# Kernel tuning notes

Hardware: AMD Instinct MI355X
Metric: run time of the kernel (lower is better)

## Reference

```python
import jax, jax.numpy as jnp
import numpy as np

N = 100_000   # nodes
E = 1_600_000 # edges (avg degree 16)
G = 1_000     # graphs in batch
IN = 3
H = 64
EPS = 1e-5    # BatchNorm eps


def setup_inputs() -> dict:
    key = jax.random.key(0)
    ks = jax.random.split(key, 16)
    x = jax.random.normal(ks[0], (N, IN), jnp.float32)
    edge_index = jax.random.randint(ks[1], (2, E), 0, N, dtype=jnp.int64)
    # sorted segment ids covering every graph (no empty segments for max-pool)
    batch = (jnp.arange(N, dtype=jnp.int64) * G) // N
    s = 0.1
    return {
        "x": x,
        "edge_index": edge_index,
        "batch": batch,
        "W0": jax.random.normal(ks[2], (IN, H), jnp.float32) * s,
        "b0": jax.random.normal(ks[3], (H,), jnp.float32) * s,
        "W_hidden": jax.random.normal(ks[4], (2, H, H), jnp.float32) * s,
        "b_hidden": jax.random.normal(ks[5], (2, H), jnp.float32) * s,
        "bn_gamma": jax.random.uniform(ks[6], (3, H), jnp.float32, 0.5, 1.5),
        "bn_beta": jax.random.normal(ks[7], (3, H), jnp.float32) * s,
        "bn_mean": jax.random.normal(ks[8], (3, H), jnp.float32) * s,
        "bn_var": jax.random.uniform(ks[9], (3, H), jnp.float32, 0.5, 1.5),
        "fc1_W": jax.random.normal(ks[10], (2 * H, 128), jnp.float32) * s,
        "fc1_b": jnp.zeros((128,), jnp.float32),
        "fc2_W": jax.random.normal(ks[11], (128, 64), jnp.float32) * s,
        "fc2_b": jnp.zeros((64,), jnp.float32),
        "fcg_W": jax.random.normal(ks[12], (64, 1), jnp.float32) * s,
        "fcg_b": jnp.zeros((1,), jnp.float32),
        "fcb_W": jax.random.normal(ks[13], (64, 1), jnp.float32) * s,
        "fcb_b": jnp.zeros((1,), jnp.float32),
    }


def _gcn_conv(h, W, b, src, dst, dinv):
    """PyG GCNConv: self-loops + symmetric deg^{-1/2} normalization."""
    hw = h @ W                                   # [N, out]
    norm = dinv[src] * dinv[dst]                 # [E]
    agg = jax.ops.segment_sum(hw[src] * norm[:, None], dst, num_segments=N)
    # self-loop contribution: norm_ii = dinv_i^2
    return agg + hw * (dinv * dinv)[:, None] + b


def reference(x, edge_index, batch, W0, b0, W_hidden, b_hidden,
              bn_gamma, bn_beta, bn_mean, bn_var,
              fc1_W, fc1_b, fc2_W, fc2_b, fcg_W, fcg_b, fcb_W, fcb_b):
    src, dst = edge_index[0], edge_index[1]
    # degree including self-loop, computed on target nodes (PyG gcn_norm)
    deg = jax.ops.segment_sum(jnp.ones((E,), x.dtype), dst, num_segments=N) + 1.0
    dinv = jax.lax.rsqrt(deg)

    h = x
    for i in range(3):
        W = W0 if i == 0 else W_hidden[i - 1]
        b = b0 if i == 0 else b_hidden[i - 1]
        hn = _gcn_conv(h, W, b, src, dst, dinv)
        # BatchNorm1d (eval mode, running stats) + ReLU; dropout = identity in eval
        hn = (hn - bn_mean[i]) * jax.lax.rsqrt(bn_var[i] + EPS) * bn_gamma[i] + bn_beta[i]
        hn = jax.nn.relu(hn)
        h = h + hn if (i > 0 and h.shape[1] == hn.shape[1]) else hn

    # segment pooling over graphs
    counts = jax.ops.segment_sum(jnp.ones((N,), h.dtype), batch, num_segments=G)
    x_mean = jax.ops.segment_sum(h, batch, num_segments=G) / counts[:, None]
    x_max = jax.ops.segment_max(h, batch, num_segments=G)
    g = jnp.concatenate([x_mean, x_max], axis=1)     # [G, 2H]

    g = jax.nn.relu(g @ fc1_W + fc1_b)
    g = jax.nn.relu(g @ fc2_W + fc2_b)
    gamma = g @ fcg_W + fcg_b
    beta = g @ fcb_W + fcb_b
    return jnp.concatenate([gamma, beta], axis=1)    # [G, 2*p_layers]
```

## Files before the change

kernel.cpp:

```cpp
#include <hip/hip_runtime.h>
#include <hip/hip_fp16.h>
#include <math.h>
#include <float.h>

#define EPSBN 1e-5f
#define NBK   200
#define CAPB  9728
#define STGB  64
#define BATCH 4096

typedef _Float16 f16x8 __attribute__((ext_vector_type(8)));
typedef float f32x4 __attribute__((ext_vector_type(4)));


__global__ void prep(const float* __restrict__ W, __half* __restrict__ Whi,
                     __half* __restrict__ Wlo, int n, int* __restrict__ cursors) {
    int i = blockIdx.x * 256 + threadIdx.x;
    if (blockIdx.x == 0 && threadIdx.x < NBK) cursors[threadIdx.x] = 0;
    if (i < n) {
        float w = W[i];
        __half hi = __float2half_rn(w);
        float rem = w - __half2float(hi);
        Whi[i] = hi;
        Wlo[i] = __float2half_rn(rem);
    }
}

__global__ void bin_edges(const int* __restrict__ src, const int* __restrict__ dst,
                          int* __restrict__ bufs, int* __restrict__ cursors,
                          int E, int N) {
    __shared__ int stage[NBK * STGB];
    __shared__ int cnt[NBK];
    __shared__ int bpos[NBK];
    int tid = threadIdx.x;
    int nb = (N + 511) >> 9;

    int chunk = (((E + gridDim.x - 1) / gridDim.x) + 3) & ~3;
    int e0 = blockIdx.x * chunk;
    int e1 = min(e0 + chunk, E);

    for (int base = e0; base < e1; base += BATCH) {
        for (int i = tid; i < NBK; i += 512) cnt[i] = 0;
        __syncthreads();

#pragma unroll
        for (int it = 0; it < 2; it++) {
            int e = base + it * 2048 + tid * 4;
            if (e + 4 <= e1) {
                int4 d4 = *(const int4*)(dst + e);
                int4 s4 = *(const int4*)(src + e);
                int dd[4] = {d4.x, d4.y, d4.z, d4.w};
                int ss[4] = {s4.x, s4.y, s4.z, s4.w};
#pragma unroll
                for (int q = 0; q < 4; q++) {
                    int d = dd[q];
                    int b = d >> 9;
                    int w = ((d & 511) << 17) | ss[q];
                    int pos = atomicAdd(&cnt[b], 1);
                    if (pos < STGB) stage[b * STGB + pos] = w;
                }
            } else {
                for (int qq = e; qq < e1 && qq < e + 4; qq++) {
                    int d = dst[qq];
                    int b = d >> 9;
                    int w = ((d & 511) << 17) | src[qq];
                    int pos = atomicAdd(&cnt[b], 1);
                    if (pos < STGB) stage[b * STGB + pos] = w;
                }
            }
        }
        __syncthreads();
        if (tid < nb) bpos[tid] = atomicAdd(&cursors[tid], min(cnt[tid], STGB));
        __syncthreads();
        int wv = tid >> 6, ln = tid & 63;
        for (int b = wv; b < nb; b += 8) {
            int c = min(cnt[b], STGB), bp = bpos[b];
            int* dstp = bufs + (size_t)b * CAPB + bp;
            for (int i = ln; i < c; i += 64)
                if (bp + i < CAPB) dstp[i] = stage[b * STGB + i];
        }
        __syncthreads();
    }
}

__global__ void __launch_bounds__(512)
build_csr(const int* __restrict__ bufs, const int* __restrict__ cursors,
          const float* __restrict__ x,
          float* __restrict__ dinv, float* __restrict__ xs,
          int* __restrict__ off0, int* __restrict__ off1,
          int* __restrict__ csr, int N) {
    __shared__ int cnt[512];
    __shared__ int pfx[512];
    __shared__ unsigned sorted[CAPB];
    int tid = threadIdx.x;
    int b = blockIdx.x;
    cnt[tid] = 0;
    __syncthreads();
    int total = min(cursors[b], CAPB);
    const int* buf = bufs + (size_t)b * CAPB;

    for (int i = tid * 4; i + 4 <= total; i += 2048) {
        int4 w4 = *(const int4*)(buf + i);
        atomicAdd(&cnt[w4.x >> 17], 1);
        atomicAdd(&cnt[w4.y >> 17], 1);
        atomicAdd(&cnt[w4.z >> 17], 1);
        atomicAdd(&cnt[w4.w >> 17], 1);
    }
    for (int i = (total & ~3) + tid; i < total; i += 512)
        atomicAdd(&cnt[buf[i] >> 17], 1);
    __syncthreads();

    int v = cnt[tid];
    pfx[tid] = v;
    __syncthreads();
    for (int off = 1; off < 512; off <<= 1) {
        int t = (tid >= off) ? pfx[tid - off] : 0;
        __syncthreads();
        pfx[tid] += t;
        __syncthreads();
    }
    int excl = pfx[tid] - v;
    int gbase = b * CAPB;
    int gi = (b << 9) + tid;
    if (gi < N) {
        float di = 1.0f / sqrtf((float)v + 1.0f);
        dinv[gi] = di;
        off0[gi] = gbase + excl;
        off1[gi] = gbase + excl + v;
        xs[gi * 3]     = x[gi * 3]     * di;
        xs[gi * 3 + 1] = x[gi * 3 + 1] * di;
        xs[gi * 3 + 2] = x[gi * 3 + 2] * di;
    }
    cnt[tid] = excl;
    __syncthreads();

    for (int i = tid * 4; i + 4 <= total; i += 2048) {
        int4 w4 = *(const int4*)(buf + i);
        int ww[4] = {w4.x, w4.y, w4.z, w4.w};
#pragma unroll
        for (int q = 0; q < 4; q++) {
            int pos = atomicAdd(&cnt[ww[q] >> 17], 1);
            sorted[pos] = (unsigned)(ww[q] & 0x1FFFF);
        }
    }
    for (int i = (total & ~3) + tid; i < total; i += 512) {
        int w = buf[i];
        int pos = atomicAdd(&cnt[w >> 17], 1);
        sorted[pos] = (unsigned)(w & 0x1FFFF);
    }
    __syncthreads();

    for (int i = tid; i < total; i += 512)
        csr[gbase + i] = (int)sorted[i];
}

__global__ void agg3(const float* __restrict__ xs, const float* __restrict__ dinv,
                     const int* __restrict__ csr,
                     const int* __restrict__ off0, const int* __restrict__ off1,
                     float* __restrict__ ax, int N) {
    int n = blockIdx.x * blockDim.x + threadIdx.x;
    if (n >= N) return;
    float a0 = xs[n * 3], a1 = xs[n * 3 + 1], a2 = xs[n * 3 + 2];
    float b0 = 0.f, b1 = 0.f, b2 = 0.f;
    int e0 = off0[n], e1 = off1[n];
    int e = e0;
    for (; e + 4 <= e1; e += 4) {
        int s0 = csr[e] * 3, s1 = csr[e + 1] * 3, s2 = csr[e + 2] * 3, s3 = csr[e + 3] * 3;
        float x00 = xs[s0], x01 = xs[s0 + 1], x02 = xs[s0 + 2];
        float x10 = xs[s1], x11 = xs[s1 + 1], x12 = xs[s1 + 2];
        float x20 = xs[s2], x21 = xs[s2 + 1], x22 = xs[s2 + 2];
        float x30 = xs[s3], x31 = xs[s3 + 1], x32 = xs[s3 + 2];
        a0 += x00 + x20; a1 += x01 + x21; a2 += x02 + x22;
        b0 += x10 + x30; b1 += x11 + x31; b2 += x12 + x32;
    }
    for (; e < e1; e++) {
        int s = csr[e] * 3;
        a0 += xs[s]; a1 += xs[s + 1]; a2 += xs[s + 2];
    }
    float di = dinv[n];
    ax[n * 3]     = (a0 + b0) * di;
    ax[n * 3 + 1] = (a1 + b1) * di;
    ax[n * 3 + 2] = (a2 + b2) * di;
}

__global__ void mm_bn(const float* __restrict__ ax, const float* __restrict__ W,
                      const float* __restrict__ b,
                      const float* __restrict__ bng, const float* __restrict__ bnb,
                      const float* __restrict__ bnm, const float* __restrict__ bnv,
                      __half* __restrict__ h, int N) {
    int t = blockIdx.x * blockDim.x + threadIdx.x;
    int n = t >> 6, f = t & 63;
    if (n < N) {
        float a = ax[n * 3] * W[f] + ax[n * 3 + 1] * W[64 + f]
                + ax[n * 3 + 2] * W[128 + f] + b[f];
        float v = (a - bnm[f]) * rsqrtf(bnv[f] + EPSBN) * bng[f] + bnb[f];
        v = fmaxf(v, 0.f);
        float other = __shfl_xor(v, 1, 64);
        if (!(f & 1)) ((__half2*)h)[t >> 1] = __floats2half2_rn(v, other);
    }
}

__global__ void __launch_bounds__(256)
mm64_mfma(const __half* __restrict__ hH, const __half* __restrict__ WhiH,
          const __half* __restrict__ WloH, const float* __restrict__ dinv,
          __half* __restrict__ hw, int N) {
    __shared__ _Float16 lds[4][16 * 68];
    const _Float16* Whi = (const _Float16*)WhiH;
    const _Float16* Wlo = (const _Float16*)WloH;
    const _Float16* hh  = (const _Float16*)hH;

    int tid = threadIdx.x;
    int lane = tid & 63;
    int wv = tid >> 6;
    int col = lane & 15;
    int q = lane >> 4;
    int gwave = blockIdx.x * 4 + wv;
    int nwaves = gridDim.x * 4;
    int ntiles = (N + 15) >> 4;

    f16x8 Bh[2][4], Bl[2][4];
#pragma unroll
    for (int t = 0; t < 2; t++)
#pragma unroll
        for (int g = 0; g < 4; g++) {
#pragma unroll
            for (int j = 0; j < 8; j++) {
                int k = t * 32 + q * 8 + j;
                Bh[t][g][j] = Whi[k * 64 + g * 16 + col];
                Bl[t][g][j] = Wlo[k * 64 + g * 16 + col];
            }
        }

    _Float16* sl = lds[wv];

    for (int tile = gwave; tile < ntiles; tile += nwaves) {
        int base = tile << 4;
        int arow = base + col;
        if (arow > N - 1) arow = N - 1;
        f32x4 acc[4] = {};
#pragma unroll
        for (int t = 0; t < 2; t++) {
            f16x8 a = *(const f16x8*)(hh + (size_t)arow * 64 + t * 32 + q * 8);
#pragma unroll
            for (int g = 0; g < 4; g++) {
                acc[g] = __builtin_amdgcn_mfma_f32_16x16x32_f16(a, Bh[t][g], acc[g], 0, 0, 0);
                acc[g] = __builtin_amdgcn_mfma_f32_16x16x32_f16(a, Bl[t][g], acc[g], 0, 0, 0);
            }
        }
#pragma unroll
        for (int r = 0; r < 4; r++) {
            int row = base + q * 4 + r;
            float di = dinv[row < N ? row : N - 1];
#pragma unroll
            for (int g = 0; g < 4; g++)
                sl[(q * 4 + r) * 68 + g * 16 + col] = (_Float16)(acc[g][r] * di);
        }
        asm volatile("s_waitcnt lgkmcnt(0)" ::: "memory");
#pragma unroll
        for (int p = 0; p < 2; p++) {
            int row = (lane >> 3) + p * 8;
            int ck = lane & 7;
            uint4 v = *(const uint4*)(sl + row * 68 + ck * 8);
            int grow = base + row;
            if (grow < N)
                *(uint4*)(hw + (size_t)grow * 64 + ck * 8) = v;
        }
        asm volatile("s_waitcnt lgkmcnt(0)" ::: "memory");
    }
}


__device__ inline void acc8(float* a, uint4 r) {
    const __half2* p = (const __half2*)&r;
#pragma unroll
    for (int j = 0; j < 4; j++) {
        float2 f = __half22float2(p[j]);
        a[2 * j] += f.x;
        a[2 * j + 1] += f.y;
    }
}

__global__ void agg_bn(const uint4* __restrict__ hw4, __half* __restrict__ h,
                       const float* __restrict__ dinv,
                       const int* __restrict__ csr,
                       const int* __restrict__ off0, const int* __restrict__ off1,
                       const float4* __restrict__ bias4,
                       const float4* __restrict__ gamma4, const float4* __restrict__ beta4,
                       const float4* __restrict__ mean4, const float4* __restrict__ var4,
                       int N) {
    int tid = threadIdx.x;
    int n = blockIdx.x * 32 + (tid >> 3);
    int f8 = tid & 7;
    if (n >= N) return;

    float a0[8], a1[8], a2[8], a3[8];
#pragma unroll
    for (int j = 0; j < 8; j++) { a0[j] = 0.f; a1[j] = 0.f; a2[j] = 0.f; a3[j] = 0.f; }
    acc8(a0, hw4[(size_t)n * 8 + f8]);

    int e0 = off0[n], e1 = off1[n];
    int e = e0;
    for (; e + 16 <= e1; e += 16) {
        int s[16];
#pragma unroll
        for (int j = 0; j < 16; j++) s[j] = csr[e + j];
        uint4 v[16];
#pragma unroll
        for (int j = 0; j < 16; j++) v[j] = hw4[(size_t)s[j] * 8 + f8];
#pragma unroll
        for (int j = 0; j < 16; j += 4) {
            acc8(a0, v[j]); acc8(a1, v[j + 1]); acc8(a2, v[j + 2]); acc8(a3, v[j + 3]);
        }
    }
    for (; e + 4 <= e1; e += 4) {
        int s0 = csr[e], s1 = csr[e + 1], s2 = csr[e + 2], s3 = csr[e + 3];
        uint4 v0 = hw4[(size_t)s0 * 8 + f8];
        uint4 v1 = hw4[(size_t)s1 * 8 + f8];
        uint4 v2 = hw4[(size_t)s2 * 8 + f8];
        uint4 v3 = hw4[(size_t)s3 * 8 + f8];
        acc8(a0, v0); acc8(a1, v1); acc8(a2, v2); acc8(a3, v3);
    }
    for (; e < e1; e++)
        acc8(a0, hw4[(size_t)csr[e] * 8 + f8]);

    float di = dinv[n];
    float4 bA = bias4[f8 * 2],  bB = bias4[f8 * 2 + 1];
    float4 gA = gamma4[f8 * 2], gB = gamma4[f8 * 2 + 1];
    float4 eA = beta4[f8 * 2],  eB = beta4[f8 * 2 + 1];
    float4 mA = mean4[f8 * 2],  mB = mean4[f8 * 2 + 1];
    float4 vA = var4[f8 * 2],   vB = var4[f8 * 2 + 1];
    float bb[8] = {bA.x, bA.y, bA.z, bA.w, bB.x, bB.y, bB.z, bB.w};
    float gg[8] = {gA.x, gA.y, gA.z, gA.w, gB.x, gB.y, gB.z, gB.w};
    float ee[8] = {eA.x, eA.y, eA.z, eA.w, eB.x, eB.y, eB.z, eB.w};
    float mm[8] = {mA.x, mA.y, mA.z, mA.w, mB.x, mB.y, mB.z, mB.w};
    float vv[8] = {vA.x, vA.y, vA.z, vA.w, vB.x, vB.y, vB.z, vB.w};

    float r[8];
#pragma unroll
    for (int j = 0; j < 8; j++) {
        float acc = (a0[j] + a1[j]) + (a2[j] + a3[j]);
        float t = (acc * di + bb[j] - mm[j]) * (1.0f / sqrtf(vv[j] + EPSBN)) * gg[j] + ee[j];
        r[j] = fmaxf(t, 0.f);
    }
    {
        uint4 hp = ((const uint4*)h)[(size_t)n * 8 + f8];
        const __half2* pp = (const __half2*)&hp;
#pragma unroll
        for (int j = 0; j < 4; j++) {
            float2 f = __half22float2(pp[j]);
            r[2 * j] += f.x;
            r[2 * j + 1] += f.y;
        }
    }
    uint4 outv;
    __half2* po = (__half2*)&outv;
#pragma unroll
    for (int j = 0; j < 4; j++) po[j] = __floats2half2_rn(r[2 * j], r[2 * j + 1]);
    ((uint4*)h)[(size_t)n * 8 + f8] = outv;
}


__device__ inline float4 h4_to_f4(uint2 r) {
    __half2 a = *(__half2*)&r.x;
    __half2 b = *(__half2*)&r.y;
    float2 fa = __half22float2(a), fb = __half22float2(b);
    return make_float4(fa.x, fa.y, fb.x, fb.y);
}

__global__ void __launch_bounds__(256)
pool_mlp(const uint2* __restrict__ h2, const int* __restrict__ batch, int N,
         const float* __restrict__ W1, const float* __restrict__ b1,
         const float* __restrict__ W2, const float* __restrict__ b2,
         const float* __restrict__ Wg, const float* __restrict__ bg,
         const float* __restrict__ Wb, const float* __restrict__ bbv,
         float* __restrict__ out) {
    __shared__ float4 ssum[256], smax[256];
    __shared__ float pooled[128];
    __shared__ float h1[128], hh2[64];
    __shared__ int range[2];
    int g = blockIdx.x;
    int tid = threadIdx.x;

    if (tid < 2) {
        int target = g + tid;
        int lo = 0, hi = N;
        while (lo < hi) {
            int mid = (lo + hi) >> 1;
            if (batch[mid] < target) lo = mid + 1; else hi = mid;
        }
        range[tid] = lo;
    }
    __syncthreads();
    int s = range[0], e = range[1];

    int f4 = tid & 15, c = tid >> 4;
    float4 sum = make_float4(0.f, 0.f, 0.f, 0.f);
    float4 mx = make_float4(-FLT_MAX, -FLT_MAX, -FLT_MAX, -FLT_MAX);
    for (int i = s + c; i < e; i += 16) {
        float4 v = h4_to_f4(h2[(size_t)i * 16 + f4]);
        sum.x += v.x; sum.y += v.y; sum.z += v.z; sum.w += v.w;
        mx.x = fmaxf(mx.x, v.x); mx.y = fmaxf(mx.y, v.y);
        mx.z = fmaxf(mx.z, v.z); mx.w = fmaxf(mx.w, v.w);
    }
    ssum[tid] = sum;
    smax[tid] = mx;
    __syncthreads();
    for (int half = 8; half >= 1; half >>= 1) {
        if (c < half) {
            int o = tid + half * 16;
            ssum[tid].x += ssum[o].x; ssum[tid].y += ssum[o].y;
            ssum[tid].z += ssum[o].z; ssum[tid].w += ssum[o].w;
            smax[tid].x = fmaxf(smax[tid].x, smax[o].x);
            smax[tid].y = fmaxf(smax[tid].y, smax[o].y);
            smax[tid].z = fmaxf(smax[tid].z, smax[o].z);
            smax[tid].w = fmaxf(smax[tid].w, smax[o].w);
        }
        __syncthreads();
    }
    if (c == 0) {
        float inv = 1.0f / (float)(e - s);
        float4 S = ssum[tid], M = smax[tid];
        pooled[f4 * 4 + 0] = S.x * inv;
        pooled[f4 * 4 + 1] = S.y * inv;
        pooled[f4 * 4 + 2] = S.z * inv;
        pooled[f4 * 4 + 3] = S.w * inv;
        pooled[64 + f4 * 4 + 0] = M.x;
        pooled[64 + f4 * 4 + 1] = M.y;
        pooled[64 + f4 * 4 + 2] = M.z;
        pooled[64 + f4 * 4 + 3] = M.w;
    }
    __syncthreads();

    if (tid < 128) {
        float acc = b1[tid];
#pragma unroll 8
        for (int k = 0; k < 128; k++) acc += pooled[k] * W1[k * 128 + tid];
        h1[tid] = fmaxf(acc, 0.0f);
    }
    __syncthreads();
    if (tid < 64) {
        float a2 = b2[tid];
#pragma unroll 8
        for (int k = 0; k < 128; k++) a2 += h1[k] * W2[k * 64 + tid];
        hh2[tid] = fmaxf(a2, 0.0f);
    }
    __syncthreads();
    if (tid < 2) {
        const float* Wv = (tid == 0) ? Wg : Wb;
        float a = (tid == 0) ? bg[0] : bbv[0];
        for (int k = 0; k < 64; k++) a += hh2[k] * Wv[k];
        out[g * 2 + tid] = a;
    }
}


extern "C" void kernel_launch(void* const* d_in, const int* in_sizes, int n_in,
                              void* d_out, int out_size, void* d_ws, size_t ws_size,
                              hipStream_t stream) {
    const float* x    = (const float*)d_in[0];
    const int*   ei   = (const int*)d_in[1];
    const int*   batch= (const int*)d_in[2];
    const float* W0   = (const float*)d_in[3];
    const float* b0   = (const float*)d_in[4];
    const float* Wh   = (const float*)d_in[5];
    const float* bh   = (const float*)d_in[6];
    const float* bng  = (const float*)d_in[7];
    const float* bnb  = (const float*)d_in[8];
    const float* bnm  = (const float*)d_in[9];
    const float* bnv  = (const float*)d_in[10];
    const float* fc1W = (const float*)d_in[11];
    const float* fc1b = (const float*)d_in[12];
    const float* fc2W = (const float*)d_in[13];
    const float* fc2b = (const float*)d_in[14];
    const float* fcgW = (const float*)d_in[15];
    const float* fcgb = (const float*)d_in[16];
    const float* fcbW = (const float*)d_in[17];
    const float* fcbb = (const float*)d_in[18];
    float* out = (float*)d_out;

    const int N = in_sizes[0] / 3;
    const int E = in_sizes[1] / 2;
    const int G = out_size / 2;
    const int* src = ei;
    const int* dst = ei + E;
    const int nb = (N + 511) >> 9;

    char* ws = (char*)d_ws;
    auto alloc = [&](size_t bytes) {
        char* p = ws;
        ws += (bytes + 255) & ~(size_t)255;
        return p;
    };
    float*  dinv    = (float*)alloc((size_t)N * 4);
    int*    off0    = (int*)alloc((size_t)N * 4);
    int*    off1    = (int*)alloc((size_t)N * 4);
    int*    csr     = (int*)alloc((size_t)NBK * CAPB * 4);
    int*    bufs    = (int*)alloc((size_t)NBK * CAPB * 4);
    int*    cursors = (int*)alloc(NBK * 4);
    float*  xs      = (float*)alloc((size_t)N * 3 * 4);
    float*  ax      = (float*)alloc((size_t)N * 3 * 4);
    __half* h       = (__half*)alloc((size_t)N * 64 * 2);
    __half* hw      = (__half*)alloc((size_t)N * 64 * 2);
    __half* whi     = (__half*)alloc(2 * 4096 * 2);
    __half* wlo     = (__half*)alloc(2 * 4096 * 2);

    const int B = 256;

    prep<<<32, 256, 0, stream>>>(Wh, whi, wlo, 8192, cursors);
    bin_edges<<<768, 512, 0, stream>>>(src, dst, bufs, cursors, E, N);
    build_csr<<<nb, 512, 0, stream>>>(bufs, cursors, x, dinv, xs, off0, off1, csr, N);

    int aggBlocks = (N + 31) / 32;

    agg3<<<(N + B - 1) / B, B, 0, stream>>>(xs, dinv, csr, off0, off1, ax, N);
    mm_bn<<<((size_t)N * 64 + B - 1) / B, B, 0, stream>>>(ax, W0, b0,
                                                          bng, bnb, bnm, bnv, h, N);
    mm64_mfma<<<784, 256, 0, stream>>>(h, whi, wlo, dinv, hw, N);
    agg_bn<<<aggBlocks, 256, 0, stream>>>((const uint4*)hw, h, dinv, csr, off0, off1,
                                          (const float4*)(bh),
                                          (const float4*)(bng + 64), (const float4*)(bnb + 64),
                                          (const float4*)(bnm + 64), (const float4*)(bnv + 64), N);
    mm64_mfma<<<784, 256, 0, stream>>>(h, whi + 4096, wlo + 4096, dinv, hw, N);
    agg_bn<<<aggBlocks, 256, 0, stream>>>((const uint4*)hw, h, dinv, csr, off0, off1,
                                          (const float4*)(bh + 64),
                                          (const float4*)(bng + 128), (const float4*)(bnb + 128),
                                          (const float4*)(bnm + 128), (const float4*)(bnv + 128), N);

    pool_mlp<<<G, 256, 0, stream>>>((const uint2*)h, batch, N,
                                    fc1W, fc1b, fc2W, fc2b,
                                    fcgW, fcgb, fcbW, fcbb, out);
}
```

Baseline: 277.3 us.

## Register-cache edge buckets, wave-shuffle scan in build_csr, 4 lanes per node in agg3

build_csr now loads each thread's slice of the bucket buffer into registers once (19 entries) and reuses it for both the histogram pass and the scatter pass. The 512-wide shared-memory Hillis-Steele scan is replaced by a wave shuffle scan plus a cross-wave sum. agg3 gives each node 4 threads that split the edge list and combine partial sums with xor shuffles, which raises parallelism for the first-layer gather. Costs are higher register pressure in build_csr and four times as many threads in agg3.

```diff
diff --git a/kernel.cpp b/kernel.cpp
--- a/kernel.cpp
+++ b/kernel.cpp
@@ -6,6 +6,7 @@
 #define EPSBN 1e-5f
 #define NBK   200
 #define CAPB  9728
+#define CEPT  19
 #define STGB  64
 #define BATCH 4096
 
@@ -90,36 +91,43 @@
           int* __restrict__ off0, int* __restrict__ off1,
           int* __restrict__ csr, int N) {
     __shared__ int cnt[512];
-    __shared__ int pfx[512];
     __shared__ unsigned sorted[CAPB];
+    __shared__ int wsum[8];
     int tid = threadIdx.x;
+    int lane = tid & 63;
+    int wid = tid >> 6;
     int b = blockIdx.x;
     cnt[tid] = 0;
     __syncthreads();
     int total = min(cursors[b], CAPB);
     const int* buf = bufs + (size_t)b * CAPB;
 
-    for (int i = tid * 4; i + 4 <= total; i += 2048) {
-        int4 w4 = *(const int4*)(buf + i);
-        atomicAdd(&cnt[w4.x >> 17], 1);
-        atomicAdd(&cnt[w4.y >> 17], 1);
-        atomicAdd(&cnt[w4.z >> 17], 1);
-        atomicAdd(&cnt[w4.w >> 17], 1);
-    }
-    for (int i = (total & ~3) + tid; i < total; i += 512)
-        atomicAdd(&cnt[buf[i] >> 17], 1);
+    int w[CEPT];
+#pragma unroll
+    for (int c = 0; c < CEPT; c++) {
+        int i = c * 512 + tid;
+        w[c] = (i < total) ? buf[i] : -1;
+    }
+#pragma unroll
+    for (int c = 0; c < CEPT; c++)
+        if (w[c] >= 0) atomicAdd(&cnt[w[c] >> 17], 1);
     __syncthreads();
 
     int v = cnt[tid];
-    pfx[tid] = v;
-    __syncthreads();
-    for (int off = 1; off < 512; off <<= 1) {
-        int t = (tid >= off) ? pfx[tid - off] : 0;
-        __syncthreads();
-        pfx[tid] += t;
-        __syncthreads();
-    }
-    int excl = pfx[tid] - v;
+    int xsc = v;
+#pragma unroll
+    for (int off = 1; off < 64; off <<= 1) {
+        int y = __shfl_up(xsc, off, 64);
+        if (lane >= off) xsc += y;
+    }
+    if (lane == 63) wsum[wid] = xsc;
+    __syncthreads();
+    int woff = 0;
+#pragma unroll
+    for (int i = 0; i < 8; i++)
+        if (i < wid) woff += wsum[i];
+    xsc += woff;
+    int excl = xsc - v;
     int gbase = b * CAPB;
     int gi = (b << 9) + tid;
     if (gi < N) {
@@ -131,22 +139,16 @@
         xs[gi * 3 + 1] = x[gi * 3 + 1] * di;
         xs[gi * 3 + 2] = x[gi * 3 + 2] * di;
     }
+    __syncthreads();
     cnt[tid] = excl;
     __syncthreads();
 
-    for (int i = tid * 4; i + 4 <= total; i += 2048) {
-        int4 w4 = *(const int4*)(buf + i);
-        int ww[4] = {w4.x, w4.y, w4.z, w4.w};
-#pragma unroll
-        for (int q = 0; q < 4; q++) {
-            int pos = atomicAdd(&cnt[ww[q] >> 17], 1);
-            sorted[pos] = (unsigned)(ww[q] & 0x1FFFF);
-        }
-    }
-    for (int i = (total & ~3) + tid; i < total; i += 512) {
-        int w = buf[i];
-        int pos = atomicAdd(&cnt[w >> 17], 1);
-        sorted[pos] = (unsigned)(w & 0x1FFFF);
+#pragma unroll
+    for (int c = 0; c < CEPT; c++) {
+        if (w[c] >= 0) {
+            int pos = atomicAdd(&cnt[w[c] >> 17], 1);
+            sorted[pos] = (unsigned)(w[c] & 0x1FFFF);
+        }
     }
     __syncthreads();
 
@@ -158,29 +160,30 @@
                      const int* __restrict__ csr,
                      const int* __restrict__ off0, const int* __restrict__ off1,
                      float* __restrict__ ax, int N) {
-    int n = blockIdx.x * blockDim.x + threadIdx.x;
+    int t = blockIdx.x * blockDim.x + threadIdx.x;
+    int n = t >> 2, sub = t & 3;
     if (n >= N) return;
-    float a0 = xs[n * 3], a1 = xs[n * 3 + 1], a2 = xs[n * 3 + 2];
-    float b0 = 0.f, b1 = 0.f, b2 = 0.f;
     int e0 = off0[n], e1 = off1[n];
-    int e = e0;
-    for (; e + 4 <= e1; e += 4) {
-        int s0 = csr[e] * 3, s1 = csr[e + 1] * 3, s2 = csr[e + 2] * 3, s3 = csr[e + 3] * 3;
-        float x00 = xs[s0], x01 = xs[s0 + 1], x02 = xs[s0 + 2];
-        float x10 = xs[s1], x11 = xs[s1 + 1], x12 = xs[s1 + 2];
-        float x20 = xs[s2], x21 = xs[s2 + 1], x22 = xs[s2 + 2];
-        float x30 = xs[s3], x31 = xs[s3 + 1], x32 = xs[s3 + 2];
-        a0 += x00 + x20; a1 += x01 + x21; a2 += x02 + x22;
-        b0 += x10 + x30; b1 += x11 + x31; b2 += x12 + x32;
-    }
-    for (; e < e1; e++) {
+    float a0 = 0.f, a1 = 0.f, a2 = 0.f;
+    int e = e0 + sub;
+    for (; e + 4 < e1; e += 8) {
+        int s  = csr[e] * 3;
+        int s2 = csr[e + 4] * 3;
+        float y0 = xs[s],      y1 = xs[s + 1],  y2 = xs[s + 2];
+        float z0 = xs[s2],     z1 = xs[s2 + 1], z2 = xs[s2 + 2];
+        a0 += y0 + z0; a1 += y1 + z1; a2 += y2 + z2;
+    }
+    if (e < e1) {
         int s = csr[e] * 3;
         a0 += xs[s]; a1 += xs[s + 1]; a2 += xs[s + 2];
     }
-    float di = dinv[n];
-    ax[n * 3]     = (a0 + b0) * di;
-    ax[n * 3 + 1] = (a1 + b1) * di;
-    ax[n * 3 + 2] = (a2 + b2) * di;
+    a0 += __shfl_xor(a0, 1, 64); a1 += __shfl_xor(a1, 1, 64); a2 += __shfl_xor(a2, 1, 64);
+    a0 += __shfl_xor(a0, 2, 64); a1 += __shfl_xor(a1, 2, 64); a2 += __shfl_xor(a2, 2, 64);
+    if (sub < 3) {
+        float di = dinv[n];
+        float sel = (sub == 0) ? a0 : (sub == 1) ? a1 : a2;
+        ax[n * 3 + sub] = (sel + xs[n * 3 + sub]) * di;
+    }
 }
 
 __global__ void mm_bn(const float* __restrict__ ax, const float* __restrict__ W,
@@ -269,7 +272,6 @@
     }
 }
 
-
 __device__ inline void acc8(float* a, uint4 r) {
     const __half2* p = (const __half2*)&r;
 #pragma unroll
@@ -358,7 +360,6 @@
     for (int j = 0; j < 4; j++) po[j] = __floats2half2_rn(r[2 * j], r[2 * j + 1]);
     ((uint4*)h)[(size_t)n * 8 + f8] = outv;
 }
-
 
 __device__ inline float4 h4_to_f4(uint2 r) {
     __half2 a = *(__half2*)&r.x;
@@ -512,7 +513,7 @@
 
     int aggBlocks = (N + 31) / 32;
 
-    agg3<<<(N + B - 1) / B, B, 0, stream>>>(xs, dinv, csr, off0, off1, ax, N);
+    agg3<<<((size_t)N * 4 + B - 1) / B, B, 0, stream>>>(xs, dinv, csr, off0, off1, ax, N);
     mm_bn<<<((size_t)N * 64 + B - 1) / B, B, 0, stream>>>(ax, W0, b0,
                                                           bng, bnb, bnm, bnv, h, N);
     mm64_mfma<<<784, 256, 0, stream>>>(h, whi, wlo, dinv, hw, N);
```

Measured after the change: 272.1 us. Within noise of the previous version (-1.9%).
